# Performance work log

Measured on AMD Instinct MI355X. Metric: run time of the kernel, lower is better.

## Reference

```python
import jax, jax.numpy as jnp
import numpy as np

N, L0, L1, D = 8, 128, 256, 512
NEG_INF = 1e12


def setup_inputs() -> dict:
    key = jax.random.key(0)
    k = jax.random.split(key, 7)
    x = jax.random.normal(k[0], (N, L0, D), dtype=jnp.float32)
    m = jax.random.normal(k[1], (N, L1, D), dtype=jnp.float32)
    mask = jax.random.randint(k[2], (N, L1), 0, 2, dtype=jnp.int32)
    # Linear(2D -> D): weight [D, 2D], bias [D]; Linear(D -> 1): weight [1, D], bias [1]
    s1 = 1.0 / np.sqrt(2 * D)
    W_w = jax.random.uniform(k[3], (D, 2 * D), jnp.float32, -s1, s1)
    W_b = jax.random.uniform(k[4], (D,), jnp.float32, -s1, s1)
    s2 = 1.0 / np.sqrt(D)
    V_w = jax.random.uniform(k[5], (1, D), jnp.float32, -s2, s2)
    V_b = jax.random.uniform(k[6], (1,), jnp.float32, -s2, s2)
    return {"x": x, "m": m, "mask": mask, "W_w": W_w, "W_b": W_b, "V_w": V_w, "V_b": V_b}


def reference(x, m, mask, W_w, W_b, V_w, V_b):
    # Split W so we never materialize the [N,L0,L1,2D] concat:
    # W([x_c, m_c]) == x @ Wx^T + m @ Wm^T (broadcast-added)
    Wx, Wm = W_w[:, :D], W_w[:, D:]
    xp = jnp.einsum('nld,ed->nle', x, Wx)           # [N,L0,D]
    mp = jnp.einsum('nld,ed->nle', m, Wm)           # [N,L1,D]
    h = jnp.tanh(xp[:, :, None, :] + mp[:, None, :, :] + W_b)  # [N,L0,L1,D]
    w = jnp.einsum('nabd,d->nab', h, V_w[0]) + V_b[0]           # [N,L0,L1]
    w = jnp.where((mask == 0)[:, None, :], -NEG_INF, w)
    w = jax.nn.softmax(w, axis=-1)
    v = jnp.einsum('nab,nbd->nad', w, m)            # sum_b w * m_c
    return v
```

## Files before the change

kernel.cpp:

```cpp
#include <hip/hip_runtime.h>
#include <hip/hip_bf16.h>

#define DD 512
#define NN 8
#define LL0 128
#define LL1 256

#define LOG2E2 2.8853900817779268f

#define PSTR ((size_t)3072 * 512)

typedef float f32x4 __attribute__((ext_vector_type(4)));
typedef __bf16 bf16x8 __attribute__((ext_vector_type(8)));

__device__ __forceinline__ float fexp2(float x) {
#if __has_builtin(__builtin_amdgcn_exp2f)
    return __builtin_amdgcn_exp2f(x);
#else
    float r; asm("v_exp_f32 %0, %1" : "=v"(r) : "v"(x)); return r;
#endif
}
__device__ __forceinline__ float frcp(float x) {
#if __has_builtin(__builtin_amdgcn_rcpf)
    return __builtin_amdgcn_rcpf(x);
#else
    float r; asm("v_rcp_f32 %0, %1" : "=v"(r) : "v"(x)); return r;
#endif
}

__device__ __forceinline__ unsigned int f2bf(float f) {
    unsigned int u = __float_as_uint(f);
    u += 0x7fffu + ((u >> 16) & 1u);
    return u >> 16;
}
__device__ __forceinline__ unsigned int pkbf(float lo, float hi) {
    return (f2bf(hi) << 16) | f2bf(lo);
}

__global__ __launch_bounds__(256, 3) void mfma_proj_kernel(
    const float* __restrict__ x, const float* __restrict__ m,
    const float* __restrict__ W, float* __restrict__ pp)
{
    __shared__ unsigned short As[64][68];
    __shared__ unsigned short Bs[64][68];

    int e0   = blockIdx.x * 64;
    int row0 = blockIdx.y * 64;
    int kb0  = blockIdx.z * 256;
    bool isx = row0 < (NN * LL0);
    int koff = isx ? 0 : DD;

    int tid  = threadIdx.x;
    int wid  = tid >> 6;
    int lane = tid & 63;
    int l15  = lane & 15, lk = lane >> 4;

    int srow = tid >> 2;
    int scol = (tid & 3) * 16;

    const float* Ap = (isx ? x + (size_t)row0 * DD
                           : m + (size_t)(row0 - NN * LL0) * DD)
                      + (size_t)srow * DD + kb0 + scol;
    const float* Bp = W + (size_t)(e0 + srow) * (2 * DD) + koff + kb0 + scol;

    float4 a0 = *(const float4*)(Ap);
    float4 a1 = *(const float4*)(Ap + 4);
    float4 a2 = *(const float4*)(Ap + 8);
    float4 a3 = *(const float4*)(Ap + 12);
    float4 b0 = *(const float4*)(Bp);
    float4 b1 = *(const float4*)(Bp + 4);
    float4 b2 = *(const float4*)(Bp + 8);
    float4 b3 = *(const float4*)(Bp + 12);

    f32x4 acc[4] = {};

    for (int kt = 0; kt < 4; ++kt) {
        if (kt) __syncthreads();
        *(uint2*)&As[srow][scol + 0]  = make_uint2(pkbf(a0.x, a0.y), pkbf(a0.z, a0.w));
        *(uint2*)&As[srow][scol + 4]  = make_uint2(pkbf(a1.x, a1.y), pkbf(a1.z, a1.w));
        *(uint2*)&As[srow][scol + 8]  = make_uint2(pkbf(a2.x, a2.y), pkbf(a2.z, a2.w));
        *(uint2*)&As[srow][scol + 12] = make_uint2(pkbf(a3.x, a3.y), pkbf(a3.z, a3.w));
        *(uint2*)&Bs[srow][scol + 0]  = make_uint2(pkbf(b0.x, b0.y), pkbf(b0.z, b0.w));
        *(uint2*)&Bs[srow][scol + 4]  = make_uint2(pkbf(b1.x, b1.y), pkbf(b1.z, b1.w));
        *(uint2*)&Bs[srow][scol + 8]  = make_uint2(pkbf(b2.x, b2.y), pkbf(b2.z, b2.w));
        *(uint2*)&Bs[srow][scol + 12] = make_uint2(pkbf(b3.x, b3.y), pkbf(b3.z, b3.w));
        if (kt < 3) {
            int ko = (kt + 1) * 64;
            a0 = *(const float4*)(Ap + ko);
            a1 = *(const float4*)(Ap + ko + 4);
            a2 = *(const float4*)(Ap + ko + 8);
            a3 = *(const float4*)(Ap + ko + 12);
            b0 = *(const float4*)(Bp + ko);
            b1 = *(const float4*)(Bp + ko + 4);
            b2 = *(const float4*)(Bp + ko + 8);
            b3 = *(const float4*)(Bp + ko + 12);
        }
        __syncthreads();

        #pragma unroll
        for (int kb = 0; kb < 2; ++kb) {
            union { unsigned int u[4]; bf16x8 v; } af;
            {
                const uint2* p = (const uint2*)&As[wid * 16 + l15][kb * 32 + lk * 8];
                uint2 lo = p[0], hi = p[1];
                af.u[0] = lo.x; af.u[1] = lo.y; af.u[2] = hi.x; af.u[3] = hi.y;
            }
            #pragma unroll
            for (int ni = 0; ni < 4; ++ni) {
                union { unsigned int u[4]; bf16x8 v; } bf;
                const uint2* p = (const uint2*)&Bs[ni * 16 + l15][kb * 32 + lk * 8];
                uint2 lo = p[0], hi = p[1];
                bf.u[0] = lo.x; bf.u[1] = lo.y; bf.u[2] = hi.x; bf.u[3] = hi.y;
                acc[ni] = __builtin_amdgcn_mfma_f32_16x16x32_bf16(af.v, bf.v, acc[ni], 0, 0, 0);
            }
        }
    }

    float* outp = pp + (size_t)blockIdx.z * PSTR;
    #pragma unroll
    for (int ni = 0; ni < 4; ++ni) {
        int col = e0 + ni * 16 + l15;
        #pragma unroll
        for (int r = 0; r < 4; ++r) {
            int row = row0 + wid * 16 + lk * 4 + r;
            outp[(size_t)row * DD + col] = acc[ni][r];
        }
    }
}

__global__ __launch_bounds__(256, 3) void logits_kernel(
    const float* __restrict__ pp, const float* __restrict__ Wb,
    const float* __restrict__ Vw, float* __restrict__ wpart)
{
    __shared__ __attribute__((aligned(16))) float xs[128][34];
    __shared__ __attribute__((aligned(16))) float ms[128][68];
    __shared__ __attribute__((aligned(16))) float vsh[128];

    int n  = blockIdx.z;
    int bt = blockIdx.x;
    int at = blockIdx.y & 3;
    int dc = blockIdx.y >> 2;
    int tid = threadIdx.x;
    int ty = tid >> 4, tx = tid & 15;

    {
        int r = tid & 31;
        int c = (tid >> 5) * 16;
        size_t base = ((size_t)(n * LL0 + at * 32) + r) * DD + dc * 128 + c;
        #pragma unroll
        for (int q = 0; q < 4; ++q) {
            float4 p0 = *(const float4*)(pp + base + q * 4);
            float4 p1 = *(const float4*)(pp + PSTR + base + q * 4);
            float4 w0 = *(const float4*)(Wb + dc * 128 + c + q * 4);
            int cc = c + q * 4;
            xs[cc + 0][r] = fexp2(LOG2E2 * (p0.x + p1.x + w0.x));
            xs[cc + 1][r] = fexp2(LOG2E2 * (p0.y + p1.y + w0.y));
            xs[cc + 2][r] = fexp2(LOG2E2 * (p0.z + p1.z + w0.z));
            xs[cc + 3][r] = fexp2(LOG2E2 * (p0.w + p1.w + w0.w));
        }
    }
    {
        int r = tid & 63;
        int c = (tid >> 6) * 32;
        size_t base = ((size_t)(NN * LL0 + n * LL1 + bt * 64) + r) * DD
                      + dc * 128 + c;
        #pragma unroll
        for (int q = 0; q < 8; ++q) {
            float4 p0 = *(const float4*)(pp + base + q * 4);
            float4 p1 = *(const float4*)(pp + PSTR + base + q * 4);
            int cc = c + q * 4;
            ms[cc + 0][r] = fexp2(LOG2E2 * (p0.x + p1.x));
            ms[cc + 1][r] = fexp2(LOG2E2 * (p0.y + p1.y));
            ms[cc + 2][r] = fexp2(LOG2E2 * (p0.z + p1.z));
            ms[cc + 3][r] = fexp2(LOG2E2 * (p0.w + p1.w));
        }
        if (tid < 32)
            *(float4*)&vsh[tid * 4] = *(const float4*)(Vw + dc * 128 + tid * 4);
    }
    __syncthreads();

    float acc[2][4] = {};

    #pragma unroll 4
    for (int kk = 0; kk < 128; kk += 4) {
        float2 xa0 = *(const float2*)&xs[kk + 0][ty * 2];
        float2 xa1 = *(const float2*)&xs[kk + 1][ty * 2];
        float2 xa2 = *(const float2*)&xs[kk + 2][ty * 2];
        float2 xa3 = *(const float2*)&xs[kk + 3][ty * 2];
        float4 mb0 = *(const float4*)&ms[kk + 0][tx * 4];
        float4 mb1 = *(const float4*)&ms[kk + 1][tx * 4];
        float4 mb2 = *(const float4*)&ms[kk + 2][tx * 4];
        float4 mb3 = *(const float4*)&ms[kk + 3][tx * 4];
        float4 vv  = *(const float4*)&vsh[kk];

        float ex[4][2] = {{xa0.x, xa0.y}, {xa1.x, xa1.y},
                          {xa2.x, xa2.y}, {xa3.x, xa3.y}};
        float fm[4][4] = {{mb0.x, mb0.y, mb0.z, mb0.w},
                          {mb1.x, mb1.y, mb1.z, mb1.w},
                          {mb2.x, mb2.y, mb2.z, mb2.w},
                          {mb3.x, mb3.y, mb3.z, mb3.w}};
        #pragma unroll
        for (int i = 0; i < 2; ++i) {
            #pragma unroll
            for (int j = 0; j < 4; ++j) {
                float D0 = fmaf(ex[0][i], fm[0][j], 1.0f);
                float D1 = fmaf(ex[1][i], fm[1][j], 1.0f);
                float D2 = fmaf(ex[2][i], fm[2][j], 1.0f);
                float D3 = fmaf(ex[3][i], fm[3][j], 1.0f);
                float P01 = D0 * D1, P23 = D2 * D3;
                float N01 = fmaf(vv.x, D1, vv.y * D0);
                float N23 = fmaf(vv.z, D3, vv.w * D2);
                float N   = fmaf(N01, P23, N23 * P01);
                acc[i][j] = fmaf(N, frcp(P01 * P23), acc[i][j]);
            }
        }
    }

    const size_t P = (size_t)NN * LL0 * LL1;
    float* wp = wpart + (size_t)dc * P
              + ((size_t)n * LL0 + at * 32 + ty * 2) * LL1 + bt * 64 + tx * 4;
    *(float4*)(wp)       = make_float4(acc[0][0], acc[0][1], acc[0][2], acc[0][3]);
    *(float4*)(wp + LL1) = make_float4(acc[1][0], acc[1][1], acc[1][2], acc[1][3]);
}

__global__ __launch_bounds__(256) void softmax_kernel(
    float* __restrict__ wpart, const int* __restrict__ mask)
{
    __shared__ float red2[4];
    const size_t P = (size_t)NN * LL0 * LL1;
    int row = blockIdx.x;
    int n = row >> 7;
    int b = threadIdx.x;
    size_t idx = (size_t)row * LL1 + b;

    float s4 = wpart[idx] + wpart[idx + P] + wpart[idx + 2 * P] + wpart[idx + 3 * P];
    float w = -2.0f * s4;

    float e = (mask[n * LL1 + b] != 0) ? __expf(w) : 0.f;
    float s = e;
    #pragma unroll
    for (int off = 32; off; off >>= 1) s += __shfl_xor(s, off);
    int wv = threadIdx.x >> 6;
    if ((threadIdx.x & 63) == 0) red2[wv] = s;
    __syncthreads();
    s = red2[0] + red2[1] + red2[2] + red2[3];

    wpart[idx] = e / s;
}

__global__ __launch_bounds__(256, 4) void vgemm_kernel(
    const float* __restrict__ wbuf, const float* __restrict__ m,
    float* __restrict__ out)
{
    __shared__ float wt[32][36];
    __shared__ float mt[32][68];

    int n  = blockIdx.z;
    int a0 = blockIdx.y * 32;
    int d0 = blockIdx.x * 64;
    int tid = threadIdx.x;
    int ty = tid >> 4, tx = tid & 15;

    const float* wrow = wbuf + ((size_t)n * LL0 + a0) * LL1;
    const float* mrow = m + (size_t)n * LL1 * DD;

    float acc[2][4] = {};
    for (int k0 = 0; k0 < LL1; k0 += 32) {
        {
            int r  = tid >> 3;
            int c4 = (tid & 7) * 4;
            float4 wv = *(const float4*)(wrow + (size_t)r * LL1 + k0 + c4);
            wt[c4 + 0][r] = wv.x; wt[c4 + 1][r] = wv.y;
            wt[c4 + 2][r] = wv.z; wt[c4 + 3][r] = wv.w;
        }
        {
            int r  = tid >> 3;
            int c8 = (tid & 7) * 8;
            const float* src = mrow + (size_t)(k0 + r) * DD + d0 + c8;
            *(float4*)&mt[r][c8]     = *(const float4*)(src);
            *(float4*)&mt[r][c8 + 4] = *(const float4*)(src + 4);
        }
        __syncthreads();
        #pragma unroll 8
        for (int kk = 0; kk < 32; ++kk) {
            float2 av = *(const float2*)&wt[kk][ty * 2];
            float4 bv = *(const float4*)&mt[kk][tx * 4];
            acc[0][0] = fmaf(av.x, bv.x, acc[0][0]);
            acc[0][1] = fmaf(av.x, bv.y, acc[0][1]);
            acc[0][2] = fmaf(av.x, bv.z, acc[0][2]);
            acc[0][3] = fmaf(av.x, bv.w, acc[0][3]);
            acc[1][0] = fmaf(av.y, bv.x, acc[1][0]);
            acc[1][1] = fmaf(av.y, bv.y, acc[1][1]);
            acc[1][2] = fmaf(av.y, bv.z, acc[1][2]);
            acc[1][3] = fmaf(av.y, bv.w, acc[1][3]);
        }
        __syncthreads();
    }
    float* op = out + ((size_t)n * LL0 + a0 + ty * 2) * DD + d0 + tx * 4;
    *(float4*)(op)      = make_float4(acc[0][0], acc[0][1], acc[0][2], acc[0][3]);
    *(float4*)(op + DD) = make_float4(acc[1][0], acc[1][1], acc[1][2], acc[1][3]);
}

extern "C" void kernel_launch(void* const* d_in, const int* in_sizes, int n_in,
                              void* d_out, int out_size, void* d_ws, size_t ws_size,
                              hipStream_t stream) {
    const float* x    = (const float*)d_in[0];
    const float* m    = (const float*)d_in[1];
    const int*   mask = (const int*)d_in[2];
    const float* W_w  = (const float*)d_in[3];
    const float* W_b  = (const float*)d_in[4];
    const float* V_w  = (const float*)d_in[5];
    const float* V_b  = (const float*)d_in[6];
    (void)V_b;
    float* out = (float*)d_out;

    float* pp    = (float*)d_ws;
    float* wpart = pp + 2 * PSTR;

    mfma_proj_kernel<<<dim3(8, 48, 2), 256, 0, stream>>>(x, m, W_w, pp);
    logits_kernel<<<dim3(4, 16, 8), 256, 0, stream>>>(pp, W_b, V_w, wpart);
    softmax_kernel<<<dim3(1024), 256, 0, stream>>>(wpart, mask);
    vgemm_kernel<<<dim3(8, 4, 8), 256, 0, stream>>>(wpart, m, out);
}
```

Measured before the change: 50.27 us.

## Fuse bias+exp into projection epilogue and softmax into PV GEMM

```diff
diff --git a/kernel.cpp b/kernel.cpp
--- a/kernel.cpp
+++ b/kernel.cpp
@@ -7,8 +7,6 @@
 #define LL1 256
 
 #define LOG2E2 2.8853900817779268f
-
-#define PSTR ((size_t)3072 * 512)
 
 typedef float f32x4 __attribute__((ext_vector_type(4)));
 typedef __bf16 bf16x8 __attribute__((ext_vector_type(8)));
@@ -39,14 +37,14 @@
 
 __global__ __launch_bounds__(256, 3) void mfma_proj_kernel(
     const float* __restrict__ x, const float* __restrict__ m,
-    const float* __restrict__ W, float* __restrict__ pp)
+    const float* __restrict__ W, const float* __restrict__ Wb,
+    float* __restrict__ exm)
 {
     __shared__ unsigned short As[64][68];
-    __shared__ unsigned short Bs[64][68];
-
-    int e0   = blockIdx.x * 64;
+    __shared__ unsigned short Bs[32][68];
+
+    int e0   = blockIdx.x * 32;
     int row0 = blockIdx.y * 64;
-    int kb0  = blockIdx.z * 256;
     bool isx = row0 < (NN * LL0);
     int koff = isx ? 0 : DD;
 
@@ -55,13 +53,13 @@
     int lane = tid & 63;
     int l15  = lane & 15, lk = lane >> 4;
 
-    int srow = tid >> 2;
-    int scol = (tid & 3) * 16;
+    int sar = tid >> 2, sac = (tid & 3) * 16;
+    int sbr = tid >> 3, sbc = (tid & 7) * 8;
 
     const float* Ap = (isx ? x + (size_t)row0 * DD
                            : m + (size_t)(row0 - NN * LL0) * DD)
-                      + (size_t)srow * DD + kb0 + scol;
-    const float* Bp = W + (size_t)(e0 + srow) * (2 * DD) + koff + kb0 + scol;
+                      + (size_t)sar * DD + sac;
+    const float* Bp = W + (size_t)(e0 + sbr) * (2 * DD) + koff + sbc;
 
     float4 a0 = *(const float4*)(Ap);
     float4 a1 = *(const float4*)(Ap + 4);
@@ -69,22 +67,18 @@
     float4 a3 = *(const float4*)(Ap + 12);
     float4 b0 = *(const float4*)(Bp);
     float4 b1 = *(const float4*)(Bp + 4);
-    float4 b2 = *(const float4*)(Bp + 8);
-    float4 b3 = *(const float4*)(Bp + 12);
-
-    f32x4 acc[4] = {};
-
-    for (int kt = 0; kt < 4; ++kt) {
+
+    f32x4 acc[2] = {};
+
+    for (int kt = 0; kt < 8; ++kt) {
         if (kt) __syncthreads();
-        *(uint2*)&As[srow][scol + 0]  = make_uint2(pkbf(a0.x, a0.y), pkbf(a0.z, a0.w));
-        *(uint2*)&As[srow][scol + 4]  = make_uint2(pkbf(a1.x, a1.y), pkbf(a1.z, a1.w));
-        *(uint2*)&As[srow][scol + 8]  = make_uint2(pkbf(a2.x, a2.y), pkbf(a2.z, a2.w));
-        *(uint2*)&As[srow][scol + 12] = make_uint2(pkbf(a3.x, a3.y), pkbf(a3.z, a3.w));
-        *(uint2*)&Bs[srow][scol + 0]  = make_uint2(pkbf(b0.x, b0.y), pkbf(b0.z, b0.w));
-        *(uint2*)&Bs[srow][scol + 4]  = make_uint2(pkbf(b1.x, b1.y), pkbf(b1.z, b1.w));
-        *(uint2*)&Bs[srow][scol + 8]  = make_uint2(pkbf(b2.x, b2.y), pkbf(b2.z, b2.w));
-        *(uint2*)&Bs[srow][scol + 12] = make_uint2(pkbf(b3.x, b3.y), pkbf(b3.z, b3.w));
-        if (kt < 3) {
+        *(uint2*)&As[sar][sac + 0]  = make_uint2(pkbf(a0.x, a0.y), pkbf(a0.z, a0.w));
+        *(uint2*)&As[sar][sac + 4]  = make_uint2(pkbf(a1.x, a1.y), pkbf(a1.z, a1.w));
+        *(uint2*)&As[sar][sac + 8]  = make_uint2(pkbf(a2.x, a2.y), pkbf(a2.z, a2.w));
+        *(uint2*)&As[sar][sac + 12] = make_uint2(pkbf(a3.x, a3.y), pkbf(a3.z, a3.w));
+        *(uint2*)&Bs[sbr][sbc + 0]  = make_uint2(pkbf(b0.x, b0.y), pkbf(b0.z, b0.w));
+        *(uint2*)&Bs[sbr][sbc + 4]  = make_uint2(pkbf(b1.x, b1.y), pkbf(b1.z, b1.w));
+        if (kt < 7) {
             int ko = (kt + 1) * 64;
             a0 = *(const float4*)(Ap + ko);
             a1 = *(const float4*)(Ap + ko + 4);
@@ -92,8 +86,6 @@
             a3 = *(const float4*)(Ap + ko + 12);
             b0 = *(const float4*)(Bp + ko);
             b1 = *(const float4*)(Bp + ko + 4);
-            b2 = *(const float4*)(Bp + ko + 8);
-            b3 = *(const float4*)(Bp + ko + 12);
         }
         __syncthreads();
 
@@ -106,7 +98,7 @@
                 af.u[0] = lo.x; af.u[1] = lo.y; af.u[2] = hi.x; af.u[3] = hi.y;
             }
             #pragma unroll
-            for (int ni = 0; ni < 4; ++ni) {
+            for (int ni = 0; ni < 2; ++ni) {
                 union { unsigned int u[4]; bf16x8 v; } bf;
                 const uint2* p = (const uint2*)&Bs[ni * 16 + l15][kb * 32 + lk * 8];
                 uint2 lo = p[0], hi = p[1];
@@ -116,21 +108,21 @@
         }
     }
 
-    float* outp = pp + (size_t)blockIdx.z * PSTR;
     #pragma unroll
-    for (int ni = 0; ni < 4; ++ni) {
+    for (int ni = 0; ni < 2; ++ni) {
         int col = e0 + ni * 16 + l15;
+        float bv = isx ? Wb[col] : 0.0f;
         #pragma unroll
         for (int r = 0; r < 4; ++r) {
             int row = row0 + wid * 16 + lk * 4 + r;
-            outp[(size_t)row * DD + col] = acc[ni][r];
+            exm[(size_t)row * DD + col] = fexp2(LOG2E2 * (acc[ni][r] + bv));
         }
     }
 }
 
 __global__ __launch_bounds__(256, 3) void logits_kernel(
-    const float* __restrict__ pp, const float* __restrict__ Wb,
-    const float* __restrict__ Vw, float* __restrict__ wpart)
+    const float* __restrict__ exm, const float* __restrict__ Vw,
+    float* __restrict__ wpart)
 {
     __shared__ __attribute__((aligned(16))) float xs[128][34];
     __shared__ __attribute__((aligned(16))) float ms[128][68];
@@ -146,33 +138,26 @@
     {
         int r = tid & 31;
         int c = (tid >> 5) * 16;
-        size_t base = ((size_t)(n * LL0 + at * 32) + r) * DD + dc * 128 + c;
+        const float* src = exm + ((size_t)(n * LL0 + at * 32) + r) * DD + dc * 128 + c;
         #pragma unroll
         for (int q = 0; q < 4; ++q) {
-            float4 p0 = *(const float4*)(pp + base + q * 4);
-            float4 p1 = *(const float4*)(pp + PSTR + base + q * 4);
-            float4 w0 = *(const float4*)(Wb + dc * 128 + c + q * 4);
+            float4 p = *(const float4*)(src + q * 4);
             int cc = c + q * 4;
-            xs[cc + 0][r] = fexp2(LOG2E2 * (p0.x + p1.x + w0.x));
-            xs[cc + 1][r] = fexp2(LOG2E2 * (p0.y + p1.y + w0.y));
-            xs[cc + 2][r] = fexp2(LOG2E2 * (p0.z + p1.z + w0.z));
-            xs[cc + 3][r] = fexp2(LOG2E2 * (p0.w + p1.w + w0.w));
+            xs[cc + 0][r] = p.x; xs[cc + 1][r] = p.y;
+            xs[cc + 2][r] = p.z; xs[cc + 3][r] = p.w;
         }
     }
     {
         int r = tid & 63;
         int c = (tid >> 6) * 32;
-        size_t base = ((size_t)(NN * LL0 + n * LL1 + bt * 64) + r) * DD
-                      + dc * 128 + c;
+        const float* src = exm + ((size_t)(NN * LL0 + n * LL1 + bt * 64) + r) * DD
+                           + dc * 128 + c;
         #pragma unroll
         for (int q = 0; q < 8; ++q) {
-            float4 p0 = *(const float4*)(pp + base + q * 4);
-            float4 p1 = *(const float4*)(pp + PSTR + base + q * 4);
+            float4 p = *(const float4*)(src + q * 4);
             int cc = c + q * 4;
-            ms[cc + 0][r] = fexp2(LOG2E2 * (p0.x + p1.x));
-            ms[cc + 1][r] = fexp2(LOG2E2 * (p0.y + p1.y));
-            ms[cc + 2][r] = fexp2(LOG2E2 * (p0.z + p1.z));
-            ms[cc + 3][r] = fexp2(LOG2E2 * (p0.w + p1.w));
+            ms[cc + 0][r] = p.x; ms[cc + 1][r] = p.y;
+            ms[cc + 2][r] = p.z; ms[cc + 3][r] = p.w;
         }
         if (tid < 32)
             *(float4*)&vsh[tid * 4] = *(const float4*)(Vw + dc * 128 + tid * 4);
@@ -223,56 +208,58 @@
     *(float4*)(wp + LL1) = make_float4(acc[1][0], acc[1][1], acc[1][2], acc[1][3]);
 }
 
-__global__ __launch_bounds__(256) void softmax_kernel(
-    float* __restrict__ wpart, const int* __restrict__ mask)
+__global__ __launch_bounds__(256, 3) void pv_kernel(
+    const float* __restrict__ wpart, const int* __restrict__ mask,
+    const float* __restrict__ m, float* __restrict__ out)
 {
-    __shared__ float red2[4];
+    __shared__ float wt[256][36];
+    __shared__ float mt[32][68];
+    __shared__ float rsum[32][9];
+    __shared__ float rinv[32];
+
     const size_t P = (size_t)NN * LL0 * LL1;
-    int row = blockIdx.x;
-    int n = row >> 7;
-    int b = threadIdx.x;
-    size_t idx = (size_t)row * LL1 + b;
-
-    float s4 = wpart[idx] + wpart[idx + P] + wpart[idx + 2 * P] + wpart[idx + 3 * P];
-    float w = -2.0f * s4;
-
-    float e = (mask[n * LL1 + b] != 0) ? __expf(w) : 0.f;
-    float s = e;
-    #pragma unroll
-    for (int off = 32; off; off >>= 1) s += __shfl_xor(s, off);
-    int wv = threadIdx.x >> 6;
-    if ((threadIdx.x & 63) == 0) red2[wv] = s;
-    __syncthreads();
-    s = red2[0] + red2[1] + red2[2] + red2[3];
-
-    wpart[idx] = e / s;
-}
-
-__global__ __launch_bounds__(256, 4) void vgemm_kernel(
-    const float* __restrict__ wbuf, const float* __restrict__ m,
-    float* __restrict__ out)
-{
-    __shared__ float wt[32][36];
-    __shared__ float mt[32][68];
-
     int n  = blockIdx.z;
     int a0 = blockIdx.y * 32;
     int d0 = blockIdx.x * 64;
     int tid = threadIdx.x;
     int ty = tid >> 4, tx = tid & 15;
 
-    const float* wrow = wbuf + ((size_t)n * LL0 + a0) * LL1;
+    {
+        int a = tid & 31;
+        int g = tid >> 5;
+        const float* wp0 = wpart + ((size_t)(n * LL0) + a0 + a) * LL1 + g * 32;
+        const int*   mk  = mask + n * LL1 + g * 32;
+        float ls = 0.f;
+        #pragma unroll
+        for (int q = 0; q < 8; ++q) {
+            float4 p0 = *(const float4*)(wp0 + q * 4);
+            float4 p1 = *(const float4*)(wp0 + P + q * 4);
+            float4 p2 = *(const float4*)(wp0 + 2 * P + q * 4);
+            float4 p3 = *(const float4*)(wp0 + 3 * P + q * 4);
+            int4   mv = *(const int4*)(mk + q * 4);
+            float w0 = mv.x ? __expf(-2.f * (p0.x + p1.x + p2.x + p3.x)) : 0.f;
+            float w1 = mv.y ? __expf(-2.f * (p0.y + p1.y + p2.y + p3.y)) : 0.f;
+            float w2 = mv.z ? __expf(-2.f * (p0.z + p1.z + p2.z + p3.z)) : 0.f;
+            float w3 = mv.w ? __expf(-2.f * (p0.w + p1.w + p2.w + p3.w)) : 0.f;
+            int b = g * 32 + q * 4;
+            wt[b + 0][a] = w0; wt[b + 1][a] = w1;
+            wt[b + 2][a] = w2; wt[b + 3][a] = w3;
+            ls += w0 + w1 + w2 + w3;
+        }
+        rsum[a][g] = ls;
+    }
+    __syncthreads();
+    if (tid < 32) {
+        float s = 0.f;
+        #pragma unroll
+        for (int g = 0; g < 8; ++g) s += rsum[tid][g];
+        rinv[tid] = frcp(s);
+    }
+    __syncthreads();
+
     const float* mrow = m + (size_t)n * LL1 * DD;
-
     float acc[2][4] = {};
     for (int k0 = 0; k0 < LL1; k0 += 32) {
-        {
-            int r  = tid >> 3;
-            int c4 = (tid & 7) * 4;
-            float4 wv = *(const float4*)(wrow + (size_t)r * LL1 + k0 + c4);
-            wt[c4 + 0][r] = wv.x; wt[c4 + 1][r] = wv.y;
-            wt[c4 + 2][r] = wv.z; wt[c4 + 3][r] = wv.w;
-        }
         {
             int r  = tid >> 3;
             int c8 = (tid & 7) * 8;
@@ -283,7 +270,7 @@
         __syncthreads();
         #pragma unroll 8
         for (int kk = 0; kk < 32; ++kk) {
-            float2 av = *(const float2*)&wt[kk][ty * 2];
+            float2 av = *(const float2*)&wt[k0 + kk][ty * 2];
             float4 bv = *(const float4*)&mt[kk][tx * 4];
             acc[0][0] = fmaf(av.x, bv.x, acc[0][0]);
             acc[0][1] = fmaf(av.x, bv.y, acc[0][1]);
@@ -296,9 +283,13 @@
         }
         __syncthreads();
     }
+
+    float r0 = rinv[ty * 2], r1 = rinv[ty * 2 + 1];
     float* op = out + ((size_t)n * LL0 + a0 + ty * 2) * DD + d0 + tx * 4;
-    *(float4*)(op)      = make_float4(acc[0][0], acc[0][1], acc[0][2], acc[0][3]);
-    *(float4*)(op + DD) = make_float4(acc[1][0], acc[1][1], acc[1][2], acc[1][3]);
+    *(float4*)(op)      = make_float4(acc[0][0] * r0, acc[0][1] * r0,
+                                      acc[0][2] * r0, acc[0][3] * r0);
+    *(float4*)(op + DD) = make_float4(acc[1][0] * r1, acc[1][1] * r1,
+                                      acc[1][2] * r1, acc[1][3] * r1);
 }
 
 extern "C" void kernel_launch(void* const* d_in, const int* in_sizes, int n_in,
@@ -314,11 +305,10 @@
     (void)V_b;
     float* out = (float*)d_out;
 
-    float* pp    = (float*)d_ws;
-    float* wpart = pp + 2 * PSTR;
-
-    mfma_proj_kernel<<<dim3(8, 48, 2), 256, 0, stream>>>(x, m, W_w, pp);
-    logits_kernel<<<dim3(4, 16, 8), 256, 0, stream>>>(pp, W_b, V_w, wpart);
-    softmax_kernel<<<dim3(1024), 256, 0, stream>>>(wpart, mask);
-    vgemm_kernel<<<dim3(8, 4, 8), 256, 0, stream>>>(wpart, m, out);
-}
+    float* exm   = (float*)d_ws;
+    float* wpart = exm + (size_t)3072 * 512;
+
+    mfma_proj_kernel<<<dim3(16, 48), 256, 0, stream>>>(x, m, W_w, W_b, exm);
+    logits_kernel<<<dim3(4, 16, 8), 256, 0, stream>>>(exm, V_w, wpart);
+    pv_kernel<<<dim3(8, 4, 8), 256, 0, stream>>>(wpart, mask, m, out);
+}
```

Result: slower. 58.37 us (+16.1%).
